# Optimization experiments

Hardware: AMD Instinct MI355X
Metric: run time of the kernel (lower is better)

The kernel has to match this reference:

```python
import jax, jax.numpy as jnp
import numpy as np

B, L, DIN, DOUT, H, N, NLAYERS, NRES, NSPECIES = 32, 2048, 5, 5, 256, 32, 4, 3, 100


def conv1d(x, w, b, pad):
    # x: (B, Cin, L), w: (Cout, Cin, K)
    y = jax.lax.conv_general_dilated(x, w, (1,), [(pad, pad)], dimension_numbers=('NCH', 'OIH', 'NCH'))
    return y + b[None, :, None]


def layer_norm_c(x, g, b):
    # LayerNorm over channel dim of (B, H, L) (matches norm(x.transpose(-1,-2)).transpose(-1,-2))
    mu = x.mean(1, keepdims=True)
    v = ((x - mu) ** 2).mean(1, keepdims=True)
    return (x - mu) / jnp.sqrt(v + 1e-5) * g[None, :, None] + b[None, :, None]


def dss_layer(x, log_dt, lam_re, lam_im, W_re, W_im, D, glu_w, glu_b):
    # Bidirectional diagonal state-space (DSS) layer, transposed layout (B, H, L).
    Bb, Hh, Ll = x.shape
    dt = jnp.exp(log_dt)                                  # (H,)
    lam = lam_re + 1j * lam_im                            # (N,) with Re(lam) < 0
    pos = jnp.arange(Ll)
    # Vandermonde: E[h,n,l] = exp(dt[h] * lam[n] * l)
    E = jnp.exp(dt[:, None, None] * lam[None, :, None] * pos[None, None, :])  # (H,N,L) complex
    W = W_re + 1j * W_im                                  # (2,H,N) fwd/bwd kernels
    k = jnp.einsum('chn,hnl->chl', W, E).real             # (2,H,L)
    zpad = jnp.zeros_like(k[0])
    k2 = jnp.concatenate([k[0], zpad], -1) + jnp.concatenate([zpad, k[1][:, ::-1]], -1)  # (H,2L)
    # FFT circular conv of length 2L -> linear conv, keep first L
    y = jnp.fft.irfft(jnp.fft.rfft(x, 2 * Ll) * jnp.fft.rfft(k2, 2 * Ll)[None], 2 * Ll)[..., :Ll]
    y = y + D[None, :, None] * x
    y = jax.nn.gelu(y, approximate=False)
    # postact GLU via position-wise linear H -> 2H
    z = jnp.einsum('oh,bhl->bol', glu_w, y) + glu_b[None, :, None]
    return z[:, :Hh] * jax.nn.sigmoid(z[:, Hh:])


def setup_inputs():
    key = jax.random.key(0)
    ks = jax.random.split(key, 20)
    g = lambda i, shape, s=0.05: jax.random.normal(ks[i], shape, jnp.float32) * s
    inp = {}
    inp['x'] = jax.random.normal(ks[0], (B, DIN, L), jnp.float32)
    inp['xs'] = jax.random.randint(ks[1], (B,), 0, NSPECIES)
    inp['enc_w'] = g(2, (H, DIN, 15))
    inp['enc_b'] = jnp.zeros((H,), jnp.float32)
    inp['res_w1'] = g(3, (NRES, H, H, 3), 0.02)
    inp['res_b1'] = jnp.zeros((NRES, H), jnp.float32)
    inp['res_w2'] = g(4, (NRES, H, H, 3), 0.02)
    inp['res_b2'] = jnp.zeros((NRES, H), jnp.float32)
    inp['log_dt'] = jax.random.uniform(ks[5], (NLAYERS, H), jnp.float32, float(np.log(1e-3)), float(np.log(1e-1)))
    inp['lam_re'] = -(0.1 + jax.random.uniform(ks[6], (NLAYERS, N), jnp.float32))
    inp['lam_im'] = jnp.broadcast_to(jnp.pi * jnp.arange(N, dtype=jnp.float32), (NLAYERS, N)) + 0.0
    inp['W_re'] = g(7, (NLAYERS, 2, H, N), 0.1)
    inp['W_im'] = g(8, (NLAYERS, 2, H, N), 0.1)
    inp['D'] = g(9, (NLAYERS, H), 1.0)
    inp['glu_w'] = g(10, (NLAYERS, 2 * H, H))
    inp['glu_b'] = jnp.zeros((NLAYERS, 2 * H), jnp.float32)
    inp['ln_g'] = jnp.ones((NLAYERS, H), jnp.float32)
    inp['ln_b'] = jnp.zeros((NLAYERS, H), jnp.float32)
    inp['dec_w'] = g(11, (DOUT, H, 15))
    inp['dec_b'] = jnp.zeros((DOUT,), jnp.float32)
    inp['sp_emb'] = g(12, (NSPECIES, H), 0.02)
    inp['h1_w'] = g(13, (128, 256)); inp['h1_b'] = jnp.zeros((128,), jnp.float32)
    inp['h2_w'] = g(14, (64, 128)); inp['h2_b'] = jnp.zeros((64,), jnp.float32)
    inp['h3_w'] = g(15, (32, 64)); inp['h3_b'] = jnp.zeros((32,), jnp.float32)
    inp['h4_w'] = g(16, (1, 32)); inp['h4_b'] = jnp.zeros((1,), jnp.float32)
    return inp


def _forward(x, xs, enc_w, enc_b, res_w1, res_b1, res_w2, res_b2, log_dt, lam_re, lam_im, W_re, W_im, D, glu_w, glu_b, ln_g, ln_b, dec_w, dec_b, sp_emb, h1_w, h1_b, h2_w, h2_b, h3_w, h3_b, h4_w, h4_b):
    h = conv1d(x, enc_w, enc_b, 7)
    for i in range(NRES):  # L1Block resnet stack (dropout/BN are identity at eval)
        r = jax.nn.relu(conv1d(h, res_w1[i], res_b1[i], 1))
        r = conv1d(r, res_w2[i], res_b2[i], 1)
        h = jax.nn.relu(r + h)
    for i in range(NLAYERS):  # post-norm DSS blocks
        z = dss_layer(h, log_dt[i], lam_re[i], lam_im[i], W_re[i], W_im[i], D[i], glu_w[i], glu_b[i])
        h = layer_norm_c(z + h, ln_g[i], ln_b[i])
    h = h + sp_emb[xs][:, :, None]  # species encoder (embed_before=False)
    seq_emb = h
    agg = h.mean(-1)  # (B, H)
    r = jax.nn.elu(agg @ h1_w.T + h1_b)
    r = jax.nn.elu(r @ h2_w.T + h2_b)
    r = jax.nn.elu(r @ h3_w.T + h3_b)
    reg_y = r @ h4_w.T + h4_b
    dec = conv1d(h, dec_w, dec_b, 7)
    return dec, seq_emb, reg_y


def reference(x, xs, enc_w, enc_b, res_w1, res_b1, res_w2, res_b2, log_dt, lam_re, lam_im, W_re, W_im, D, glu_w, glu_b, ln_g, ln_b, dec_w, dec_b, sp_emb, h1_w, h1_b, h2_w, h2_b, h3_w, h3_b, h4_w, h4_b):
    return _forward(x, xs, enc_w, enc_b, res_w1, res_b1, res_w2, res_b2, log_dt, lam_re, lam_im, W_re, W_im, D, glu_w, glu_b, ln_g, ln_b, dec_w, dec_b, sp_emb, h1_w, h1_b, h2_w, h2_b, h3_w, h3_b, h4_w, h4_b)
```

## Files before the change

kernel.cpp:

```cpp
#include <hip/hip_runtime.h>
#include <math.h>

#define B 32
#define L 2048
#define DIN 5
#define DOUT 5
#define H 256
#define NST 32
#define NLAYERS 4
#define NRES 3
#define CHUNK 128
#define NCH 16
#define LSEQ (B*H*L)

typedef __attribute__((ext_vector_type(8))) _Float16 half8;
typedef __attribute__((ext_vector_type(4))) float f32x4;

__device__ __forceinline__ float gelu_exact(float v) {
    return 0.5f * v * (1.0f + erff(v * 0.7071067811865475f));
}
#define SWZ(r) ((((r) ^ ((r) >> 2)) & 3))
#define LDIDX(l, c) ((l)*281 + ((c)>>5)*35 + ((c)&31))

__global__ void k_wenc(const float* __restrict__ ew, _Float16* __restrict__ wenc) {
    int idx = blockIdx.x*256 + threadIdx.x;
    if (idx >= 256*96) return;
    int o = idx / 96, kk = idx % 96;
    int ci = kk >> 4, k = kk & 15;
    float v = (ci < DIN && k < 15) ? ew[(o*DIN + ci)*15 + k] : 0.f;
    wenc[idx] = (_Float16)v;
}

__global__ __launch_bounds__(256) void k_enc(const float* __restrict__ x,
        const _Float16* __restrict__ wenc, const float* __restrict__ bias,
        _Float16* __restrict__ out) {
    __shared__ _Float16 a_lds[3*128*32];
    __shared__ _Float16 b_lds[3*128*32];
    const int tid = threadIdx.x;
    const int mbase = blockIdx.x * 128;
    const int oh = blockIdx.y;
    const int b = mbase >> 11;
    const int lbase = mbase & 2047;
    const int lane = tid & 63;
    const int w = tid >> 6;
    const int wm = (w >> 1) * 64, wn = (w & 1) * 64;
    const int fr = lane & 15, kg = lane >> 4;

    #pragma unroll
    for (int i = 0; i < 6; ++i) {
        int g = i*256 + tid;
        int r = g / 12, rem = g % 12;
        int ks = rem >> 2, q = rem & 3;
        int kk0 = ks*32 + q*8;
        int ci = kk0 >> 4, k0 = kk0 & 15;
        half8 va;
        #pragma unroll
        for (int e = 0; e < 8; ++e) {
            int k = k0 + e;
            int l = lbase + r - 7 + k;
            float v = (ci < DIN && k < 15 && l >= 0 && l < L)
                        ? x[((size_t)(b*DIN + ci))*L + l] : 0.f;
            va[e] = (_Float16)v;
        }
        *(half8*)&a_lds[ks*4096 + r*32 + ((q ^ SWZ(r))*8)] = va;
        uint4 vb = *(const uint4*)&wenc[(size_t)(oh*128 + r)*96 + kk0];
        *(uint4*)&b_lds[ks*4096 + r*32 + ((q ^ SWZ(r))*8)] = vb;
    }
    __syncthreads();
    f32x4 acc[4][4];
    #pragma unroll
    for (int i = 0; i < 4; ++i)
        #pragma unroll
        for (int j = 0; j < 4; ++j)
            #pragma unroll
            for (int k = 0; k < 4; ++k) acc[i][j][k] = 0.f;
    #pragma unroll
    for (int ks = 0; ks < 3; ++ks) {
        half8 af[4], bfr[4];
        #pragma unroll
        for (int mf = 0; mf < 4; ++mf) {
            int ra = wm + mf*16 + fr;
            af[mf] = *(const half8*)&a_lds[ks*4096 + ra*32 + ((kg ^ SWZ(ra))*8)];
        }
        #pragma unroll
        for (int nf = 0; nf < 4; ++nf) {
            int rb = wn + nf*16 + fr;
            bfr[nf] = *(const half8*)&b_lds[ks*4096 + rb*32 + ((kg ^ SWZ(rb))*8)];
        }
        #pragma unroll
        for (int mf = 0; mf < 4; ++mf)
            #pragma unroll
            for (int nf = 0; nf < 4; ++nf)
                acc[mf][nf] = __builtin_amdgcn_mfma_f32_16x16x32_f16(af[mf], bfr[nf], acc[mf][nf], 0, 0, 0);
    }
    #pragma unroll
    for (int nf = 0; nf < 4; ++nf) {
        int o = oh*128 + wn + nf*16 + fr;
        float bo = bias[o];
        #pragma unroll
        for (int mf = 0; mf < 4; ++mf)
            #pragma unroll
            for (int rg = 0; rg < 4; ++rg) {
                size_t m = (size_t)mbase + wm + mf*16 + kg*4 + rg;
                out[m*256 + o] = (_Float16)(acc[mf][nf][rg] + bo);
            }
    }
}

__global__ void k_wpack(const float* __restrict__ w1, const float* __restrict__ w2,
                        _Float16* __restrict__ wpk) {
    int idx = blockIdx.x*256 + threadIdx.x;
    if (idx >= NRES*2*3*65536) return;
    int ci = idx & 255;
    int o  = (idx >> 8) & 255;
    int k  = (idx >> 16) % 3;
    int cv = idx / (3*65536);
    const float* src = (cv & 1) ? w2 : w1;
    wpk[idx] = (_Float16)src[(((cv>>1)*H + o)*H + ci)*3 + k];
}

__global__ __launch_bounds__(256) void k_t_cf16(const _Float16* __restrict__ in,
        _Float16* __restrict__ out) {
    __shared__ float t[64][65];
    int tid = threadIdx.x;
    int l0 = blockIdx.x*64, c0 = blockIdx.y*64, b = blockIdx.z;
    #pragma unroll
    for (int i = 0; i < 16; ++i) {
        int idx = i*256 + tid;
        int l = idx >> 6, c = idx & 63;
        t[c][l] = (float)in[((size_t)b*L + l0 + l)*256 + c0 + c];
    }
    __syncthreads();
    #pragma unroll
    for (int i = 0; i < 16; ++i) {
        int idx = i*256 + tid;
        int c = idx >> 6, l = idx & 63;
        out[((size_t)(b*H + c0 + c))*L + l0 + l] = (_Float16)t[c][l];
    }
}

__global__ __launch_bounds__(256) void k_t16(const _Float16* __restrict__ in,
                                             _Float16* __restrict__ out) {
    __shared__ float t[64][65];
    int tid = threadIdx.x;
    int l0 = blockIdx.x*64, c0 = blockIdx.y*64, b = blockIdx.z;
    #pragma unroll
    for (int i = 0; i < 16; ++i) {
        int idx = i*256 + tid;
        int c = idx >> 6, l = idx & 63;
        t[c][l] = (float)in[((size_t)(b*H + c0 + c))*L + l0 + l];
    }
    __syncthreads();
    #pragma unroll
    for (int i = 0; i < 16; ++i) {
        int idx = i*256 + tid;
        int l = idx >> 6, c = idx & 63;
        out[((size_t)b*L + l0 + l)*256 + c0 + c] = (_Float16)t[c][l];
    }
}

template<bool RESID>
__global__ __launch_bounds__(256, 2) void k_cv3(const _Float16* __restrict__ xin,
        const _Float16* __restrict__ wpk, const float* __restrict__ bias,
        const _Float16* __restrict__ resid, _Float16* __restrict__ out) {
    __shared__ _Float16 a_lds[128*32];
    __shared__ _Float16 b_lds[256*32];
    __shared__ float    ep[32*256];
    const int tid = threadIdx.x;
    const int mbase = blockIdx.x * 128;
    const int lane = tid & 63;
    const int w = tid >> 6;
    const int wm = (w >> 1) * 64, wo = (w & 1) * 128;
    const int fr = lane & 15, kg = lane >> 4;

    const int r0s = tid >> 2, q0 = tid & 3;
    const int sq = SWZ(r0s);
    const int awA0 = r0s*32 + ((q0 ^ sq) * 8);
    const int awA1 = (64 + r0s)*32 + ((q0 ^ SWZ(64 + r0s)) * 8);

    f32x4 acc[4][8];
    #pragma unroll
    for (int i = 0; i < 4; ++i)
        #pragma unroll
        for (int j = 0; j < 8; ++j)
            #pragma unroll
            for (int k = 0; k < 4; ++k) acc[i][j][k] = 0.f;

    uint4 pa0, pa1, pb[4];
    auto loadstep = [&](int kk, uint4& a0, uint4& a1, uint4 (&bb)[4]) {
        const int koff = kk >> 3, cic = kk & 7;
        const int cb = cic*32 + q0*8;
        {
            int m = mbase + r0s;
            int ll = (m & (L-1)) + koff - 1;
            a0 = (ll >= 0 && ll < L) ? *(const uint4*)&xin[((size_t)(m + koff - 1))*256 + cb]
                                     : make_uint4(0,0,0,0);
            int m1 = mbase + 64 + r0s;
            int l1 = (m1 & (L-1)) + koff - 1;
            a1 = (l1 >= 0 && l1 < L) ? *(const uint4*)&xin[((size_t)(m1 + koff - 1))*256 + cb]
                                     : make_uint4(0,0,0,0);
        }
        #pragma unroll
        for (int u = 0; u < 4; ++u)
            bb[u] = *(const uint4*)&wpk[((size_t)(koff*256 + u*64 + r0s))*256 + cb];
    };
    loadstep(0, pa0, pa1, pb);
    for (int kk = 0; kk < 24; ++kk) {
        __syncthreads();
        *(uint4*)&a_lds[awA0] = pa0;
        *(uint4*)&a_lds[awA1] = pa1;
        #pragma unroll
        for (int u = 0; u < 4; ++u)
            *(uint4*)&b_lds[(u*64 + r0s)*32 + ((q0 ^ sq)*8)] = pb[u];
        uint4 na0 = make_uint4(0,0,0,0), na1 = na0, nb[4] = {na0, na0, na0, na0};
        if (kk < 23) loadstep(kk+1, na0, na1, nb);
        __syncthreads();
        half8 af[4];
        #pragma unroll
        for (int mf = 0; mf < 4; ++mf) {
            int ra = wm + mf*16 + fr;
            af[mf] = *(const half8*)&a_lds[ra*32 + ((kg ^ SWZ(ra)) * 8)];
        }
        #pragma unroll
        for (int nf = 0; nf < 8; ++nf) {
            int rb = wo + nf*16 + fr;
            half8 bfr = *(const half8*)&b_lds[rb*32 + ((kg ^ SWZ(rb)) * 8)];
            #pragma unroll
            for (int mf = 0; mf < 4; ++mf)
                acc[mf][nf] = __builtin_amdgcn_mfma_f32_16x16x32_f16(af[mf], bfr, acc[mf][nf], 0, 0, 0);
        }
        pa0 = na0; pa1 = na1;
        #pragma unroll
        for (int u = 0; u < 4; ++u) pb[u] = nb[u];
    }
    float bo8[8];
    #pragma unroll
    for (int nf = 0; nf < 8; ++nf) bo8[nf] = bias[wo + nf*16 + fr];
    const int er = tid >> 3, eoc = (tid & 7) * 32;
    #pragma unroll
    for (int mf = 0; mf < 4; ++mf) {
        __syncthreads();
        #pragma unroll
        for (int nf = 0; nf < 8; ++nf) {
            int o = wo + nf*16 + fr;
            int srb = (w >> 1)*16 + kg*4;
            #pragma unroll
            for (int rg = 0; rg < 4; ++rg)
                ep[(srb + rg)*256 + o] = acc[mf][nf][rg] + bo8[nf];
        }
        __syncthreads();
        size_t m = (size_t)mbase + mf*16 + (er < 16 ? er : 48 + er);
        #pragma unroll
        for (int u = 0; u < 4; ++u) {
            float4 v0 = *(float4*)&ep[er*256 + eoc + u*8];
            float4 v1 = *(float4*)&ep[er*256 + eoc + u*8 + 4];
            float vv[8] = {v0.x, v0.y, v0.z, v0.w, v1.x, v1.y, v1.z, v1.w};
            if (RESID) {
                half8 rv = *(const half8*)&resid[m*256 + eoc + u*8];
                #pragma unroll
                for (int e = 0; e < 8; ++e) vv[e] += (float)rv[e];
            }
            half8 hv;
            #pragma unroll
            for (int e = 0; e < 8; ++e) hv[e] = (_Float16)fmaxf(vv[e], 0.f);
            *(half8*)&out[m*256 + eoc + u*8] = hv;
        }
    }
}

__global__ __launch_bounds__(128) void k_wzp(const float* __restrict__ log_dt,
        const float* __restrict__ lam_re, const float* __restrict__ lam_im,
        _Float16* __restrict__ zp, float4* __restrict__ zwbuf, int layer) {
    int hh = blockIdx.x;
    int t = threadIdx.x;
    int dn = t >> 1, c = t & 1, dir = dn >> 5, n = dn & 31;
    float dt = expf(log_dt[layer*H + hh]);
    float a  = dt * lam_re[layer*NST + n];
    float bi = dt * lam_im[layer*NST + n];
    float er = expf(a);
    float zre = er * cosf(bi), zim = er * sinf(bi);
    if (c == 0 && dir == 0) {
        float eC = expf(a * (float)CHUNK);
        float s, co; sincosf(bi * (float)CHUNK, &s, &co);
        zwbuf[hh*NST + n] = make_float4(zre, zim, eC*co, eC*s);
    }
    _Float16* dst = &zp[(size_t)hh*16384 + t*128];
    float cr = 1.f, ci = 0.f;
    for (int p = 0; p < 128; ++p) {
        float val = c ? ci : cr;
        dst[dir ? p : (127 - p)] = (_Float16)val;
        float nr = cr*zre - ci*zim;
        float ni = cr*zim + ci*zre;
        cr = nr; ci = ni;
    }
}

__global__ __launch_bounds__(128) void k_wkern(const float* __restrict__ log_dt,
        const float* __restrict__ lam_re, const float* __restrict__ lam_im,
        const float* __restrict__ W_re, const float* __restrict__ W_im,
        const float* __restrict__ Dv, const float* __restrict__ gw,
        _Float16* __restrict__ wbig, _Float16* __restrict__ wg, int layer) {
    __shared__ float kf[128], kb[128];
    __shared__ float E[128*129];
    const int hh = blockIdx.x;
    const int t = threadIdx.x;
    float dt = expf(log_dt[layer*H + hh]);
    float skf = 0.f, skb = 0.f;
    for (int n = 0; n < 32; ++n) {
        float a  = dt * lam_re[layer*NST + n];
        float bi = dt * lam_im[layer*NST + n];
        float wfr = W_re[((layer*2+0)*H + hh)*NST + n];
        float wfi = W_im[((layer*2+0)*H + hh)*NST + n];
        float wbr = W_re[((layer*2+1)*H + hh)*NST + n];
        float wbi = W_im[((layer*2+1)*H + hh)*NST + n];
        float e0 = expf(a*t), s0, c0; sincosf(bi*t, &s0, &c0);
        float zr0 = e0*c0, zi0 = e0*s0;
        skf = fmaf(wfr, zr0, skf) - wfi*zi0;
        skb = fmaf(wbr, zr0, skb) - wbi*zi0;
        float e1 = expf(a*(t+1)), s1, c1; sincosf(bi*(t+1), &s1, &c1);
        float zr1 = e1*c1, zi1 = e1*s1;
        E[t*129 + n]      = wfr*zr1 - wfi*zi1;
        E[t*129 + 32 + n] = -(wfr*zi1 + wfi*zr1);
        float e2 = expf(a*(127-t)), s2, c2; sincosf(bi*(127-t), &s2, &c2);
        float zr2 = e2*c2, zi2 = e2*s2;
        E[t*129 + 64 + n] = wbr*zr2 - wbi*zi2;
        E[t*129 + 96 + n] = -(wbr*zi2 + wbi*zr2);
    }
    kf[t] = skf + ((t == 0) ? Dv[layer*H + hh] : 0.f);
    kb[t] = skb;
    __syncthreads();
    _Float16* dst = &wbig[(size_t)hh*32768];
    for (int idx = t; idx < 128*256; idx += 128) {
        int tt = idx >> 8, k = idx & 255;
        float v;
        if (k < 128) v = (k <= tt) ? kf[tt - k] : kb[k - tt - 1];
        else         v = E[tt*129 + (k - 128)];
        dst[idx] = (_Float16)v;
    }
    const float* gsrc = &gw[(size_t)layer*131072 + (size_t)hh*512];
    _Float16* gdst = &wg[(size_t)hh*512];
    for (int j = t; j < 512; j += 128) gdst[j] = (_Float16)gsrc[j];
}

__global__ void k_wdec(const float* __restrict__ dw, _Float16* __restrict__ wdk) {
    int idx = blockIdx.x*256 + threadIdx.x;
    if (idx >= 15*16*256) return;
    int cfull = idx & 255;
    int o = (idx >> 8) & 15;
    int k = idx >> 12;
    float v = (o < DOUT) ? dw[(o*H + cfull)*15 + k] : 0.f;
    int cc = cfull >> 5, cl = cfull & 31;
    int cq = cl >> 3, cb = cl & 7;
    wdk[cc*7680 + (k*16 + o)*32 + ((cq ^ SWZ(o))*8) + cb] = (_Float16)v;
}

__global__ __launch_bounds__(256, 4) void k_dss(const _Float16* __restrict__ hm16,
        const _Float16* __restrict__ zp, const _Float16* __restrict__ wbig,
        const float4* __restrict__ zwb, _Float16* __restrict__ y16, int layer) {
    __shared__ _Float16 xbuf[4*32*32];
    __shared__ _Float16 bbuf[2*128*32];
    __shared__ float    sbuf[32*128];
    _Float16* sb16 = (_Float16*)sbuf;

    const int tid = threadIdx.x;
    const int hh = blockIdx.x;
    const int b0 = blockIdx.y * 2;
    const int lane = tid & 63;
    const int w = tid >> 6;
    const int wn = w * 32;
    const int fr = lane & 15, kg = lane >> 4;

    #pragma unroll
    for (int i = 0; i < 2; ++i) {
        int g = i*256 + tid;
        int m = g >> 4, gi = g & 15;
        int kc = gi >> 2, q = gi & 3;
        uint4 v = *(const uint4*)&hm16[((size_t)((b0 + (m>>4))*H + hh))*L
                                       + (m&15)*128 + kc*32 + q*8];
        *(uint4*)&xbuf[kc*1024 + m*32 + ((q ^ SWZ(m))*8)] = v;
    }

    f32x4 acc1[2][2];
    #pragma unroll
    for (int i = 0; i < 2; ++i)
        #pragma unroll
        for (int j = 0; j < 2; ++j)
            #pragma unroll
            for (int k = 0; k < 4; ++k) acc1[i][j][k] = 0.f;
    const _Float16* zb = &zp[(size_t)hh*16384];
    const int gr0 = tid >> 2, gq0 = tid & 3;
    const int gr1 = 64 + gr0;
    const int bw0 = gr0*32 + ((gq0 ^ SWZ(gr0))*8);
    const int bw1 = gr1*32 + ((gq0 ^ SWZ(gr1))*8);
    uint4 pb0 = *(const uint4*)&zb[gr0*128 + gq0*8];
    uint4 pb1 = *(const uint4*)&zb[gr1*128 + gq0*8];
    *(uint4*)&bbuf[bw0] = pb0;
    *(uint4*)&bbuf[bw1] = pb1;
    pb0 = *(const uint4*)&zb[gr0*128 + 32 + gq0*8];
    pb1 = *(const uint4*)&zb[gr1*128 + 32 + gq0*8];
    __syncthreads();
    for (int kc = 0; kc < 4; ++kc) {
        if (kc < 3) {
            *(uint4*)&bbuf[((kc+1)&1)*4096 + bw0] = pb0;
            *(uint4*)&bbuf[((kc+1)&1)*4096 + bw1] = pb1;
            if (kc < 2) {
                pb0 = *(const uint4*)&zb[gr0*128 + (kc+2)*32 + gq0*8];
                pb1 = *(const uint4*)&zb[gr1*128 + (kc+2)*32 + gq0*8];
            }
        }
        half8 af[2], bf2[2];
        #pragma unroll
        for (int mf = 0; mf < 2; ++mf) {
            int ra = mf*16 + fr;
            af[mf] = *(const half8*)&xbuf[kc*1024 + ra*32 + ((kg ^ SWZ(ra))*8)];
        }
        #pragma unroll
        for (int nf = 0; nf < 2; ++nf) {
            int rb = wn + nf*16 + fr;
            bf2[nf] = *(const half8*)&bbuf[(kc&1)*4096 + rb*32 + ((kg ^ SWZ(rb))*8)];
        }
        #pragma unroll
        for (int mf = 0; mf < 2; ++mf)
            #pragma unroll
            for (int nf = 0; nf < 2; ++nf)
                acc1[mf][nf] = __builtin_amdgcn_mfma_f32_16x16x32_f16(af[mf], bf2[nf], acc1[mf][nf], 0, 0, 0);
        __syncthreads();
    }
    #pragma unroll
    for (int mf = 0; mf < 2; ++mf)
        #pragma unroll
        for (int nf = 0; nf < 2; ++nf)
            #pragma unroll
            for (int rg = 0; rg < 4; ++rg)
                sbuf[(mf*16 + kg*4 + rg)*128 + wn + nf*16 + fr] = acc1[mf][nf][rg];
    __syncthreads();

    {
        int b_loc = tid >> 6, dn = tid & 63;
        if (b_loc < 2) {
            int dir = dn >> 5, n = dn & 31;
            float4 z4 = zwb[hh*NST + n];
            float zcre = z4.z, zcim = z4.w;
            int q1 = n >> 3, e1 = n & 7;
            float pre = 0.f, pim = 0.f;
            for (int s = 0; s < NCH; ++s) {
                int ch = dir ? (NCH - 1 - s) : s;
                int m = b_loc*16 + ch;
                bbuf[(dir*2 + 0)*1024 + m*32 + ((q1 ^ SWZ(m))*8) + e1] = (_Float16)pre;
                bbuf[(dir*2 + 1)*1024 + m*32 + ((q1 ^ SWZ(m))*8) + e1] = (_Float16)pim;
                float cre = sbuf[m*128 + dn*2];
                float cim = sbuf[m*128 + dn*2 + 1];
                float nre = fmaf(zcre, pre, fmaf(-zcim, pim, cre));
                float nim = fmaf(zcre, pim, fmaf(zcim, pre, cim));
                pre = nre; pim = nim;
            }
        }
    }
    __syncthreads();

    f32x4 acc3[2][2];
    #pragma unroll
    for (int i = 0; i < 2; ++i)
        #pragma unroll
        for (int j = 0; j < 2; ++j)
            #pragma unroll
            for (int k = 0; k < 4; ++k) acc3[i][j][k] = 0.f;
    const _Float16* wb = &wbig[(size_t)hh*32768];
    pb0 = *(const uint4*)&wb[gr0*256 + gq0*8];
    pb1 = *(const uint4*)&wb[gr1*256 + gq0*8];
    *(uint4*)&sb16[bw0] = pb0;
    *(uint4*)&sb16[bw1] = pb1;
    pb0 = *(const uint4*)&wb[gr0*256 + 32 + gq0*8];
    pb1 = *(const uint4*)&wb[gr1*256 + 32 + gq0*8];
    __syncthreads();
    for (int kc = 0; kc < 8; ++kc) {
        if (kc < 7) {
            *(uint4*)&sb16[((kc+1)&1)*4096 + bw0] = pb0;
            *(uint4*)&sb16[((kc+1)&1)*4096 + bw1] = pb1;
            if (kc < 6) {
                pb0 = *(const uint4*)&wb[gr0*256 + (kc+2)*32 + gq0*8];
                pb1 = *(const uint4*)&wb[gr1*256 + (kc+2)*32 + gq0*8];
            }
        }
        half8 af[2], bf2[2];
        #pragma unroll
        for (int mf = 0; mf < 2; ++mf) {
            int ra = mf*16 + fr;
            af[mf] = (kc < 4)
                ? *(const half8*)&xbuf[kc*1024 + ra*32 + ((kg ^ SWZ(ra))*8)]
                : *(const half8*)&bbuf[(kc-4)*1024 + ra*32 + ((kg ^ SWZ(ra))*8)];
        }
        #pragma unroll
        for (int nf = 0; nf < 2; ++nf) {
            int rb = wn + nf*16 + fr;
            bf2[nf] = *(const half8*)&sb16[(kc&1)*4096 + rb*32 + ((kg ^ SWZ(rb))*8)];
        }
        #pragma unroll
        for (int mf = 0; mf < 2; ++mf)
            #pragma unroll
            for (int nf = 0; nf < 2; ++nf)
                acc3[mf][nf] = __builtin_amdgcn_mfma_f32_16x16x32_f16(af[mf], bf2[nf], acc3[mf][nf], 0, 0, 0);
        __syncthreads();
    }
    _Float16* yst = sb16;
    #pragma unroll
    for (int mf = 0; mf < 2; ++mf) {
        #pragma unroll
        for (int rg = 0; rg < 4; ++rg) {
            int m = mf*16 + kg*4 + rg;
            #pragma unroll
            for (int nf = 0; nf < 2; ++nf) {
                int t = wn + nf*16 + fr;
                yst[m*136 + t] = (_Float16)gelu_exact(acc3[mf][nf][rg]);
            }
        }
    }
    __syncthreads();
    {
        int r = tid >> 3, tc = (tid & 7) * 16;
        size_t gb = ((size_t)((b0 + (r>>4))*H + hh))*L + (r&15)*128;
        *(half8*)&y16[gb + tc]     = *(half8*)&yst[r*136 + tc];
        *(half8*)&y16[gb + tc + 8] = *(half8*)&yst[r*136 + tc + 8];
    }
}

__global__ __launch_bounds__(256) void k_glu16(const _Float16* __restrict__ yt,
        const _Float16* __restrict__ wg, const float* __restrict__ bias,
        _Float16* __restrict__ zc) {
    __shared__ _Float16 a_lds[128*32];
    __shared__ _Float16 b_lds[128*32];
    __shared__ float    ep[32*64];
    const int tid = threadIdx.x;
    const int mbase = blockIdx.x * 128;
    const int o0 = blockIdx.y * 64;
    const int lane = tid & 63;
    const int w = tid >> 6;
    const int wm = (w >> 1) * 64, wn = (w & 1) * 32;
    const int fr = lane & 15, kg = lane >> 4;
    const int r0s = tid >> 2, q0 = tid & 3;
    const int r1s = 64 + r0s;
    const int aw0 = r0s*32 + ((q0 ^ SWZ(r0s)) * 8);
    const int aw1 = r1s*32 + ((q0 ^ SWZ(r1s)) * 8);
    const int og0 = o0 + r0s;
    const int og1 = 256 + o0 + r0s;

    f32x4 accg[4][2], accs[4][2];
    #pragma unroll
    for (int i = 0; i < 4; ++i)
        #pragma unroll
        for (int j = 0; j < 2; ++j)
            #pragma unroll
            for (int k = 0; k < 4; ++k) { accg[i][j][k] = 0.f; accs[i][j][k] = 0.f; }

    uint4 pa0, pa1, pb0, pb1;
    auto loadstep = [&](int kc, uint4& a0, uint4& a1, uint4& b0, uint4& b1) {
        const int cb = kc*32 + q0*8;
        a0 = *(const uint4*)&yt[((size_t)(mbase + r0s))*256 + cb];
        a1 = *(const uint4*)&yt[((size_t)(mbase + r1s))*256 + cb];
        b0 = *(const uint4*)&wg[((size_t)og0)*256 + cb];
        b1 = *(const uint4*)&wg[((size_t)og1)*256 + cb];
    };
    loadstep(0, pa0, pa1, pb0, pb1);
    for (int kc = 0; kc < 8; ++kc) {
        __syncthreads();
        *(uint4*)&a_lds[aw0] = pa0;
        *(uint4*)&a_lds[aw1] = pa1;
        *(uint4*)&b_lds[aw0] = pb0;
        *(uint4*)&b_lds[aw1] = pb1;
        uint4 na0 = make_uint4(0,0,0,0), na1 = na0, nb0 = na0, nb1 = na0;
        if (kc < 7) loadstep(kc+1, na0, na1, nb0, nb1);
        __syncthreads();
        half8 af[4], bg[2], bs[2];
        #pragma unroll
        for (int mf = 0; mf < 4; ++mf) {
            int ra = wm + mf*16 + fr;
            af[mf] = *(const half8*)&a_lds[ra*32 + ((kg ^ SWZ(ra)) * 8)];
        }
        #pragma unroll
        for (int nf = 0; nf < 2; ++nf) {
            int rb = wn + nf*16 + fr;
            bg[nf] = *(const half8*)&b_lds[rb*32 + ((kg ^ SWZ(rb)) * 8)];
            int rb2 = 64 + rb;
            bs[nf] = *(const half8*)&b_lds[rb2*32 + ((kg ^ SWZ(rb2)) * 8)];
        }
        #pragma unroll
        for (int mf = 0; mf < 4; ++mf)
            #pragma unroll
            for (int nf = 0; nf < 2; ++nf) {
                accg[mf][nf] = __builtin_amdgcn_mfma_f32_16x16x32_f16(af[mf], bg[nf], accg[mf][nf], 0, 0, 0);
                accs[mf][nf] = __builtin_amdgcn_mfma_f32_16x16x32_f16(af[mf], bs[nf], accs[mf][nf], 0, 0, 0);
            }
        pa0 = na0; pa1 = na1; pb0 = nb0; pb1 = nb1;
    }
    float b0v[2], b1v[2];
    #pragma unroll
    for (int nf = 0; nf < 2; ++nf) {
        int o = o0 + wn + nf*16 + fr;
        b0v[nf] = bias[o]; b1v[nf] = bias[256 + o];
    }
    const int er = tid >> 3, eoc = (tid & 7) * 8;
    #pragma unroll
    for (int mf = 0; mf < 4; ++mf) {
        __syncthreads();
        #pragma unroll
        for (int nf = 0; nf < 2; ++nf) {
            int ol = wn + nf*16 + fr;
            int srb = (w >> 1)*16 + kg*4;
            #pragma unroll
            for (int rg = 0; rg < 4; ++rg) {
                float g = accg[mf][nf][rg] + b0v[nf];
                float s = accs[mf][nf][rg] + b1v[nf];
                ep[(srb + rg)*64 + ol] = g / (1.f + expf(-s));
            }
        }
        __syncthreads();
        size_t m = (size_t)mbase + mf*16 + (er < 16 ? er : 48 + er);
        float4 v0 = *(float4*)&ep[er*64 + eoc];
        float4 v1 = *(float4*)&ep[er*64 + eoc + 4];
        half8 hv;
        hv[0]=(_Float16)v0.x; hv[1]=(_Float16)v0.y; hv[2]=(_Float16)v0.z; hv[3]=(_Float16)v0.w;
        hv[4]=(_Float16)v1.x; hv[5]=(_Float16)v1.y; hv[6]=(_Float16)v1.z; hv[7]=(_Float16)v1.w;
        *(half8*)&zc[m*256 + o0 + eoc] = hv;
    }
}

template<bool SP>
__global__ __launch_bounds__(256) void k_ln2(const _Float16* __restrict__ zc,
        _Float16* __restrict__ hm, const float* __restrict__ g, const float* __restrict__ bb,
        const int* __restrict__ xs, const float* __restrict__ emb,
        float* __restrict__ outseq) {
    __shared__ float tl[8992];
    int tid = threadIdx.x;
    int b = blockIdx.y;
    int l0 = blockIdx.x * 32;
    for (int j = tid; j < 1024; j += 256) {
        int c = j >> 2, l8 = (j & 3) * 8;
        half8 v = *(const half8*)&hm[((size_t)(b*H + c))*L + l0 + l8];
        #pragma unroll
        for (int e = 0; e < 8; ++e) tl[LDIDX(l8 + e, c)] = (float)v[e];
    }
    __syncthreads();
    int r = tid >> 3, p = tid & 7;
    float v[32];
    float sum = 0.f, ss = 0.f;
    const _Float16* zrow = &zc[((size_t)(b*L + l0 + r))*256 + p*32];
    #pragma unroll
    for (int q = 0; q < 4; ++q) {
        half8 z8 = *(const half8*)&zrow[q*8];
        #pragma unroll
        for (int i = 0; i < 8; ++i) {
            float hv = tl[LDIDX(r, p*32 + q*8 + i)];
            float vv = (float)z8[i] + hv;
            v[q*8+i] = vv;
            sum += vv; ss = fmaf(vv, vv, ss);
        }
    }
    sum += __shfl_xor(sum, 1); ss += __shfl_xor(ss, 1);
    sum += __shfl_xor(sum, 2); ss += __shfl_xor(ss, 2);
    sum += __shfl_xor(sum, 4); ss += __shfl_xor(ss, 4);
    float mu = sum * (1.f/256.f);
    float var = ss * (1.f/256.f) - mu*mu;
    float rs = rsqrtf(var + 1e-5f);
    int sp = SP ? xs[b] : 0;
    #pragma unroll
    for (int q = 0; q < 32; ++q) {
        int c = p*32 + q;
        float val = (v[q] - mu) * rs * g[c] + bb[c];
        if (SP) val += emb[sp*H + c];
        tl[LDIDX(r, c)] = val;
    }
    __syncthreads();
    for (int j = tid; j < 1024; j += 256) {
        int c = j >> 2, l8 = (j & 3) * 8;
        float fv[8];
        half8 hv;
        #pragma unroll
        for (int e = 0; e < 8; ++e) {
            fv[e] = tl[LDIDX(l8 + e, c)];
            hv[e] = (_Float16)fv[e];
        }
        *(half8*)&hm[((size_t)(b*H + c))*L + l0 + l8] = hv;
        if (SP) {
            *(float4*)&outseq[((size_t)(b*H + c))*L + l0 + l8] = make_float4(fv[0],fv[1],fv[2],fv[3]);
            *(float4*)&outseq[((size_t)(b*H + c))*L + l0 + l8 + 4] = make_float4(fv[4],fv[5],fv[6],fv[7]);
        }
    }
}

__global__ __launch_bounds__(128) void k_dec(const _Float16* __restrict__ ht,
        const _Float16* __restrict__ wdk, const float* __restrict__ bias,
        float* __restrict__ outdec) {
    __shared__ _Float16 a_lds[160*32];
    __shared__ _Float16 b_lds[15*16*32];
    const int tid = threadIdx.x;
    const int mbase = blockIdx.x * 128;
    const int b = mbase >> 11;
    const int lbase = mbase & 2047;
    const int lane = tid & 63;
    const int w = tid >> 6;
    const int fr = lane & 15, kg = lane >> 4;
    const int rs = tid >> 2, q0 = tid & 3;
    f32x4 acc[4];
    #pragma unroll
    for (int i = 0; i < 4; ++i)
        #pragma unroll
        for (int k = 0; k < 4; ++k) acc[i][k] = 0.f;
    for (int cc = 0; cc < 8; ++cc) {
        __syncthreads();
        #pragma unroll
        for (int ps = 0; ps < 5; ++ps) {
            int r = ps*32 + rs;
            if (r < 142) {
                int l = lbase - 7 + r;
                uint4 v = (l >= 0 && l < L) ? *(const uint4*)&ht[((size_t)(b*L + l))*256 + cc*32 + q0*8]
                                            : make_uint4(0,0,0,0);
                *(uint4*)&a_lds[r*32 + ((q0 ^ SWZ(r))*8)] = v;
            }
        }
        for (int jj = tid; jj < 960; jj += 128)
            *(uint4*)&b_lds[jj*8] = *(const uint4*)&wdk[cc*7680 + jj*8];
        __syncthreads();
        #pragma unroll
        for (int k = 0; k < 15; ++k) {
            half8 bfr = *(const half8*)&b_lds[(k*16 + fr)*32 + ((kg ^ SWZ(fr))*8)];
            #pragma unroll
            for (int mf = 0; mf < 4; ++mf) {
                int ra = w*64 + mf*16 + fr + k;
                half8 af = *(const half8*)&a_lds[ra*32 + ((kg ^ SWZ(ra))*8)];
                acc[mf] = __builtin_amdgcn_mfma_f32_16x16x32_f16(af, bfr, acc[mf], 0, 0, 0);
            }
        }
    }
    if (fr < DOUT) {
        float bo = bias[fr];
        #pragma unroll
        for (int mf = 0; mf < 4; ++mf)
            #pragma unroll
            for (int rg = 0; rg < 4; ++rg) {
                int m = mbase + w*64 + mf*16 + kg*4 + rg;
                outdec[((size_t)(b*DOUT + fr))*L + (m & 2047)] = acc[mf][rg] + bo;
            }
    }
}

__global__ __launch_bounds__(256) void k_agg(const _Float16* __restrict__ h, float* __restrict__ agg) {
    __shared__ float red[256];
    int bc = blockIdx.x;
    int tid = threadIdx.x;
    half8 v = *(const half8*)&h[(size_t)bc*L + tid*8];
    float s = 0.f;
    #pragma unroll
    for (int e = 0; e < 8; ++e) s += (float)v[e];
    red[tid] = s; __syncthreads();
    for (int k = 128; k > 0; k >>= 1) {
        if (tid < k) red[tid] += red[tid+k];
        __syncthreads();
    }
    if (tid == 0) agg[bc] = red[0] * (1.f/(float)L);
}

__global__ __launch_bounds__(128) void k_mlp(const float* __restrict__ agg,
        const float* __restrict__ w1, const float* __restrict__ b1,
        const float* __restrict__ w2, const float* __restrict__ b2,
        const float* __restrict__ w3, const float* __restrict__ b3,
        const float* __restrict__ w4, const float* __restrict__ b4,
        float* __restrict__ outreg) {
    __shared__ float a0[256], r1[128], r2[64], r3[32];
    int b = blockIdx.x, tid = threadIdx.x;
    a0[tid] = agg[b*256 + tid];
    a0[tid+128] = agg[b*256 + tid + 128];
    __syncthreads();
    {
        float s = b1[tid];
        for (int k = 0; k < 256; ++k) s = fmaf(w1[tid*256+k], a0[k], s);
        r1[tid] = s > 0.f ? s : expm1f(s);
    }
    __syncthreads();
    if (tid < 64) {
        float s = b2[tid];
        for (int k = 0; k < 128; ++k) s = fmaf(w2[tid*128+k], r1[k], s);
        r2[tid] = s > 0.f ? s : expm1f(s);
    }
    __syncthreads();
    if (tid < 32) {
        float s = b3[tid];
        for (int k = 0; k < 64; ++k) s = fmaf(w3[tid*64+k], r2[k], s);
        r3[tid] = s > 0.f ? s : expm1f(s);
    }
    __syncthreads();
    if (tid == 0) {
        float s = b4[0];
        for (int k = 0; k < 32; ++k) s = fmaf(w4[k], r3[k], s);
        outreg[b] = s;
    }
}

extern "C" void kernel_launch(void* const* d_in, const int* in_sizes, int n_in,
                              void* d_out, int out_size, void* d_ws, size_t ws_size,
                              hipStream_t stream) {
    const float* x      = (const float*)d_in[0];
    const int*   xs     = (const int*)d_in[1];
    const float* enc_w  = (const float*)d_in[2];
    const float* enc_b  = (const float*)d_in[3];
    const float* res_w1 = (const float*)d_in[4];
    const float* res_b1 = (const float*)d_in[5];
    const float* res_w2 = (const float*)d_in[6];
    const float* res_b2 = (const float*)d_in[7];
    const float* log_dt = (const float*)d_in[8];
    const float* lam_re = (const float*)d_in[9];
    const float* lam_im = (const float*)d_in[10];
    const float* W_re   = (const float*)d_in[11];
    const float* W_im   = (const float*)d_in[12];
    const float* Dv     = (const float*)d_in[13];
    const float* glu_w  = (const float*)d_in[14];
    const float* glu_b  = (const float*)d_in[15];
    const float* ln_g   = (const float*)d_in[16];
    const float* ln_b   = (const float*)d_in[17];
    const float* dec_w  = (const float*)d_in[18];
    const float* dec_b  = (const float*)d_in[19];
    const float* sp_emb = (const float*)d_in[20];
    const float* h1_w = (const float*)d_in[21]; const float* h1_b = (const float*)d_in[22];
    const float* h2_w = (const float*)d_in[23]; const float* h2_b = (const float*)d_in[24];
    const float* h3_w = (const float*)d_in[25]; const float* h3_b = (const float*)d_in[26];
    const float* h4_w = (const float*)d_in[27]; const float* h4_b = (const float*)d_in[28];

    float* ws   = (float*)d_ws;
    _Float16* hm16 = (_Float16*)ws;
    float* t1   = ws + (size_t)LSEQ;
    float* t2   = ws + (size_t)2*LSEQ;
    _Float16* xb  = (_Float16*)t1;
    _Float16* xa  = (_Float16*)t1 + (size_t)LSEQ;
    _Float16* wpk = (_Float16*)t2;
    _Float16* yt   = (_Float16*)t1;
    _Float16* wbig = (_Float16*)t1 + (size_t)LSEQ;
    _Float16* zp   = wbig + (size_t)H*32768;
    _Float16* y16  = (_Float16*)t2;
    _Float16* zc16 = (_Float16*)t2;
    _Float16* dect = (_Float16*)t1;
    float* tail = ws + (size_t)3*LSEQ;
    _Float16* wg  = (_Float16*)tail;
    float4* zwb = (float4*)(tail + 65536);
    float* aggb = tail + 65536 + 32768;
    _Float16* wdk = (_Float16*)(aggb + 8192);
    _Float16* wenc = wdk + 61440;

    float* outdec = (float*)d_out;
    float* outseq = outdec + B*DOUT*L;
    float* outreg = outseq + (size_t)LSEQ;

    k_wenc<<<96, 256, 0, stream>>>(enc_w, wenc);
    k_enc<<<dim3(B*L/128, 2), 256, 0, stream>>>(x, wenc, enc_b, xa);

    k_wpack<<<(NRES*2*3*65536 + 255)/256, 256, 0, stream>>>(res_w1, res_w2, wpk);
    for (int r = 0; r < NRES; ++r) {
        k_cv3<false><<<B*L/128, 256, 0, stream>>>(
            xa, wpk + (size_t)(r*2+0)*3*65536, res_b1 + r*H, nullptr, xb);
        k_cv3<true><<<B*L/128, 256, 0, stream>>>(
            xb, wpk + (size_t)(r*2+1)*3*65536, res_b2 + r*H, xa, xa);
    }
    k_t_cf16<<<dim3(L/64, H/64, B), 256, 0, stream>>>(xa, hm16);

    for (int i = 0; i < NLAYERS; ++i) {
        k_wzp<<<H, 128, 0, stream>>>(log_dt, lam_re, lam_im, zp, zwb, i);
        k_wkern<<<H, 128, 0, stream>>>(log_dt, lam_re, lam_im, W_re, W_im, Dv, glu_w,
                                       wbig, wg, i);
        k_dss<<<dim3(H, 16), 256, 0, stream>>>(hm16, zp, wbig, zwb, y16, i);
        k_t16<<<dim3(L/64, H/64, B), 256, 0, stream>>>(y16, yt);
        k_glu16<<<dim3(B*L/128, 4), 256, 0, stream>>>(yt, wg, glu_b + i*512, zc16);
        if (i < NLAYERS - 1)
            k_ln2<false><<<dim3(L/32, B), 256, 0, stream>>>(zc16, hm16, ln_g + i*H, ln_b + i*H,
                                                            nullptr, nullptr, nullptr);
        else
            k_ln2<true><<<dim3(L/32, B), 256, 0, stream>>>(zc16, hm16, ln_g + i*H, ln_b + i*H,
                                                           xs, sp_emb, outseq);
    }

    k_agg<<<B*H, 256, 0, stream>>>(hm16, aggb);
    k_mlp<<<B, 128, 0, stream>>>(aggb, h1_w, h1_b, h2_w, h2_b, h3_w, h3_b, h4_w, h4_b, outreg);
    k_t16<<<dim3(L/64, H/64, B), 256, 0, stream>>>(hm16, dect);
    k_wdec<<<(15*16*256 + 255)/256, 256, 0, stream>>>(dec_w, wdk);
    k_dec<<<B*L/128, 128, 0, stream>>>(dect, wdk, dec_b, outdec);
}
```

Baseline: 1.092 ms.

## Vectorize transposes, merge zp setup into k_wkern, use fast erf GELU

The two fp16 transpose kernels now move data as 8-wide half vectors instead of scalar elements, which cuts the number of global memory transactions. The k_wzp setup kernel is folded into k_wkern, removing one launch per layer. The exact erf in the DSS GELU epilogue is replaced by the Abramowitz-Stegun polynomial with __expf, which is cheaper but introduces an approximation error of about 1e-7. The LDS writes in the transpose use a strided pattern that may cause bank conflicts.

Result: no change. 1.079 ms (-1.2%).

```diff
diff --git a/kernel.cpp b/kernel.cpp
--- a/kernel.cpp
+++ b/kernel.cpp
@@ -18,6 +18,16 @@
 
 __device__ __forceinline__ float gelu_exact(float v) {
     return 0.5f * v * (1.0f + erff(v * 0.7071067811865475f));
+}
+__device__ __forceinline__ float gelu_fast(float v) {
+    float x = v * 0.7071067811865475f;
+    float ax = fabsf(x);
+    float t = 1.f / fmaf(0.3275911f, ax, 1.f);
+    float poly = t*(0.254829592f + t*(-0.284496736f + t*(1.421413741f +
+                 t*(-1.453152027f + t*1.061405429f))));
+    float e = __expf(-ax*ax);
+    float erfv = copysignf(1.f - poly*e, x);
+    return 0.5f * v * (1.f + erfv);
 }
 #define SWZ(r) ((((r) ^ ((r) >> 2)) & 3))
 #define LDIDX(l, c) ((l)*281 + ((c)>>5)*35 + ((c)&31))
@@ -125,17 +135,22 @@
     int tid = threadIdx.x;
     int l0 = blockIdx.x*64, c0 = blockIdx.y*64, b = blockIdx.z;
     #pragma unroll
-    for (int i = 0; i < 16; ++i) {
-        int idx = i*256 + tid;
-        int l = idx >> 6, c = idx & 63;
-        t[c][l] = (float)in[((size_t)b*L + l0 + l)*256 + c0 + c];
-    }
-    __syncthreads();
-    #pragma unroll
-    for (int i = 0; i < 16; ++i) {
-        int idx = i*256 + tid;
-        int c = idx >> 6, l = idx & 63;
-        out[((size_t)(b*H + c0 + c))*L + l0 + l] = (_Float16)t[c][l];
+    for (int i = 0; i < 2; ++i) {
+        int g = i*256 + tid;
+        int c8 = (g & 7) * 8, l = g >> 3;
+        half8 v = *(const half8*)&in[((size_t)b*L + l0 + l)*256 + c0 + c8];
+        #pragma unroll
+        for (int e = 0; e < 8; ++e) t[c8 + e][l] = (float)v[e];
+    }
+    __syncthreads();
+    #pragma unroll
+    for (int i = 0; i < 2; ++i) {
+        int g = i*256 + tid;
+        int l8 = (g & 7) * 8, c = g >> 3;
+        half8 hv;
+        #pragma unroll
+        for (int e = 0; e < 8; ++e) hv[e] = (_Float16)t[c][l8 + e];
+        *(half8*)&out[((size_t)(b*H + c0 + c))*L + l0 + l8] = hv;
     }
 }
 
@@ -145,17 +160,22 @@
     int tid = threadIdx.x;
     int l0 = blockIdx.x*64, c0 = blockIdx.y*64, b = blockIdx.z;
     #pragma unroll
-    for (int i = 0; i < 16; ++i) {
-        int idx = i*256 + tid;
-        int c = idx >> 6, l = idx & 63;
-        t[c][l] = (float)in[((size_t)(b*H + c0 + c))*L + l0 + l];
-    }
-    __syncthreads();
-    #pragma unroll
-    for (int i = 0; i < 16; ++i) {
-        int idx = i*256 + tid;
-        int l = idx >> 6, c = idx & 63;
-        out[((size_t)b*L + l0 + l)*256 + c0 + c] = (_Float16)t[c][l];
+    for (int i = 0; i < 2; ++i) {
+        int g = i*256 + tid;
+        int l8 = (g & 7) * 8, c = g >> 3;
+        half8 v = *(const half8*)&in[((size_t)(b*H + c0 + c))*L + l0 + l8];
+        #pragma unroll
+        for (int e = 0; e < 8; ++e) t[c][l8 + e] = (float)v[e];
+    }
+    __syncthreads();
+    #pragma unroll
+    for (int i = 0; i < 2; ++i) {
+        int g = i*256 + tid;
+        int c8 = (g & 7) * 8, l = g >> 3;
+        half8 hv;
+        #pragma unroll
+        for (int e = 0; e < 8; ++e) hv[e] = (_Float16)t[c8 + e][l];
+        *(half8*)&out[((size_t)b*L + l0 + l)*256 + c0 + c8] = hv;
     }
 }
 
@@ -268,38 +288,12 @@
     }
 }
 
-__global__ __launch_bounds__(128) void k_wzp(const float* __restrict__ log_dt,
-        const float* __restrict__ lam_re, const float* __restrict__ lam_im,
-        _Float16* __restrict__ zp, float4* __restrict__ zwbuf, int layer) {
-    int hh = blockIdx.x;
-    int t = threadIdx.x;
-    int dn = t >> 1, c = t & 1, dir = dn >> 5, n = dn & 31;
-    float dt = expf(log_dt[layer*H + hh]);
-    float a  = dt * lam_re[layer*NST + n];
-    float bi = dt * lam_im[layer*NST + n];
-    float er = expf(a);
-    float zre = er * cosf(bi), zim = er * sinf(bi);
-    if (c == 0 && dir == 0) {
-        float eC = expf(a * (float)CHUNK);
-        float s, co; sincosf(bi * (float)CHUNK, &s, &co);
-        zwbuf[hh*NST + n] = make_float4(zre, zim, eC*co, eC*s);
-    }
-    _Float16* dst = &zp[(size_t)hh*16384 + t*128];
-    float cr = 1.f, ci = 0.f;
-    for (int p = 0; p < 128; ++p) {
-        float val = c ? ci : cr;
-        dst[dir ? p : (127 - p)] = (_Float16)val;
-        float nr = cr*zre - ci*zim;
-        float ni = cr*zim + ci*zre;
-        cr = nr; ci = ni;
-    }
-}
-
 __global__ __launch_bounds__(128) void k_wkern(const float* __restrict__ log_dt,
         const float* __restrict__ lam_re, const float* __restrict__ lam_im,
         const float* __restrict__ W_re, const float* __restrict__ W_im,
         const float* __restrict__ Dv, const float* __restrict__ gw,
-        _Float16* __restrict__ wbig, _Float16* __restrict__ wg, int layer) {
+        _Float16* __restrict__ wbig, _Float16* __restrict__ wg,
+        _Float16* __restrict__ zp, float4* __restrict__ zwbuf, int layer) {
     __shared__ float kf[128], kb[128];
     __shared__ float E[128*129];
     const int hh = blockIdx.x;
@@ -340,6 +334,27 @@
     const float* gsrc = &gw[(size_t)layer*131072 + (size_t)hh*512];
     _Float16* gdst = &wg[(size_t)hh*512];
     for (int j = t; j < 512; j += 128) gdst[j] = (_Float16)gsrc[j];
+    {
+        int dn = t >> 1, c = t & 1, dir = dn >> 5, n = dn & 31;
+        float a  = dt * lam_re[layer*NST + n];
+        float bi = dt * lam_im[layer*NST + n];
+        float er = expf(a);
+        float zre = er * cosf(bi), zim = er * sinf(bi);
+        if (c == 0 && dir == 0) {
+            float eC = expf(a * (float)CHUNK);
+            float s, co; sincosf(bi * (float)CHUNK, &s, &co);
+            zwbuf[hh*NST + n] = make_float4(zre, zim, eC*co, eC*s);
+        }
+        _Float16* zdst = &zp[(size_t)hh*16384 + t*128];
+        float cr = 1.f, ci = 0.f;
+        for (int p = 0; p < 128; ++p) {
+            float val = c ? ci : cr;
+            zdst[dir ? p : (127 - p)] = (_Float16)val;
+            float nr = cr*zre - ci*zim;
+            float ni = cr*zim + ci*zre;
+            cr = nr; ci = ni;
+        }
+    }
 }
 
 __global__ void k_wdec(const float* __restrict__ dw, _Float16* __restrict__ wdk) {
@@ -511,7 +526,7 @@
             #pragma unroll
             for (int nf = 0; nf < 2; ++nf) {
                 int t = wn + nf*16 + fr;
-                yst[m*136 + t] = (_Float16)gelu_exact(acc3[mf][nf][rg]);
+                yst[m*136 + t] = (_Float16)gelu_fast(acc3[mf][nf][rg]);
             }
         }
     }
@@ -861,9 +876,8 @@
     k_t_cf16<<<dim3(L/64, H/64, B), 256, 0, stream>>>(xa, hm16);
 
     for (int i = 0; i < NLAYERS; ++i) {
-        k_wzp<<<H, 128, 0, stream>>>(log_dt, lam_re, lam_im, zp, zwb, i);
         k_wkern<<<H, 128, 0, stream>>>(log_dt, lam_re, lam_im, W_re, W_im, Dv, glu_w,
-                                       wbig, wg, i);
+                                       wbig, wg, zp, zwb, i);
         k_dss<<<dim3(H, 16), 256, 0, stream>>>(hm16, zp, wbig, zwb, y16, i);
         k_t16<<<dim3(L/64, H/64, B), 256, 0, stream>>>(y16, yt);
         k_glu16<<<dim3(B*L/128, 4), 256, 0, stream>>>(yt, wg, glu_b + i*512, zc16);
```
